# Kernel tuning notes

Hardware: AMD Instinct MI355X
Metric: run time of the kernel (lower is better)

The kernel has to match this reference:

```python
import jax, jax.numpy as jnp
import numpy as np

NUM_HEADS = 16
HEAD_DIM = 64
HIDDEN = NUM_HEADS * HEAD_DIM
LN_EPS = 1e-6


def setup_inputs() -> dict:
    key = jax.random.key(0)
    ks = jax.random.split(key, 5)
    B, T, H = 2, 2048, HIDDEN
    s = 1.0 / np.sqrt(H)
    return {
        "h": jax.random.normal(ks[0], (B, T, H), jnp.float32),
        "Wq": jax.random.normal(ks[1], (H, H), jnp.float32) * s,
        "bq": jnp.zeros((H,), jnp.float32),
        "Wk": jax.random.normal(ks[2], (H, H), jnp.float32) * s,
        "bk": jnp.zeros((H,), jnp.float32),
        "Wv": jax.random.normal(ks[3], (H, H), jnp.float32) * s,
        "bv": jnp.zeros((H,), jnp.float32),
        "Wo": jax.random.normal(ks[4], (H, H), jnp.float32) * s,
        "bo": jnp.zeros((H,), jnp.float32),
        "gamma": jnp.ones((H,), jnp.float32),
        "beta": jnp.zeros((H,), jnp.float32),
    }


def _split_heads(x):
    B, T, H = x.shape
    return x.reshape(B, T, NUM_HEADS, HEAD_DIM).transpose(0, 2, 1, 3)  # [B,h,T,d]


def reference(h, Wq, bq, Wk, bk, Wv, bv, Wo, bo, gamma, beta):
    # QKV projections (nn.Linear: x @ W^T + b)
    Q = _split_heads(h @ Wq.T + bq)
    K = _split_heads(h @ Wk.T + bk)
    V = _split_heads(h @ Wv.T + bv)
    scale = HEAD_DIM ** -0.5
    scores = jnp.einsum("bhqd,bhkd->bhqk", Q, K) * scale  # [B,h,T,T]
    attn = jax.nn.softmax(scores, axis=-1)
    ctx = jnp.einsum("bhqk,bhkd->bhqd", attn, V)          # [B,h,T,d]
    B, _, T, _ = ctx.shape
    ctx = ctx.transpose(0, 2, 1, 3).reshape(B, T, HIDDEN)
    out = ctx @ Wo.T + bo + h  # dropout is identity at eval
    # LayerNorm(eps=1e-6)
    mu = out.mean(-1, keepdims=True)
    var = jnp.mean((out - mu) ** 2, -1, keepdims=True)
    return (out - mu) * jax.lax.rsqrt(var + LN_EPS) * gamma + beta
```

## Files before the change

### kernel.cpp

```cpp
#include <hip/hip_runtime.h>
#include <hip/hip_bf16.h>

#define NH   16
#define HD   64
#define HID  1024
#define TSEQ 2048
#define BATCH 2
#define KSCALE 0.18033688011112042f

typedef __attribute__((ext_vector_type(4))) float f32x4;
typedef __attribute__((ext_vector_type(8))) short s16x8;
typedef __attribute__((ext_vector_type(4))) short s16x4;
typedef __attribute__((ext_vector_type(8))) _Float16 f16x8;

__device__ __forceinline__ unsigned short f2bf(float f) {
  union { float f; unsigned int u; } v; v.f = f;
  unsigned int r = v.u + 0x7fffu + ((v.u >> 16) & 1u);
  return (unsigned short)(r >> 16);
}
__device__ __forceinline__ float bf2f(unsigned short b) {
  union { unsigned int u; float f; } v; v.u = ((unsigned int)b) << 16; return v.f;
}

__device__ __forceinline__ void async_cp16(const unsigned short* g, unsigned short* l) {
  __builtin_amdgcn_global_load_lds(
      (const __attribute__((address_space(1))) unsigned int*)g,
      (__attribute__((address_space(3))) unsigned int*)l, 16, 0, 0);
}

__global__ __launch_bounds__(256) void cast_all_k(
    const float* __restrict__ h,
    const float* __restrict__ w0, const float* __restrict__ w1,
    const float* __restrict__ w2, const float* __restrict__ w3,
    unsigned short* __restrict__ hb, unsigned short* __restrict__ wbase) {
  int i = blockIdx.x * 256 + threadIdx.x;
  const float* src; unsigned short* dst; int idx; float sc = 1.f;
  if (i < 1048576) { src = h; dst = hb; idx = i; }
  else {
    int idx4 = i - 1048576;
    int w = idx4 >> 18;
    idx = idx4 & 262143;
    src = (w == 0) ? w0 : (w == 1) ? w1 : (w == 2) ? w2 : w3;
    dst = wbase + (size_t)(idx4 - idx) * 4;
    if (w == 1) sc = KSCALE;
  }
  float4 v = ((const float4*)src)[idx];
  ushort4 o;
  o.x = f2bf(v.x * sc); o.y = f2bf(v.y * sc); o.z = f2bf(v.z * sc); o.w = f2bf(v.w * sc);
  ((ushort4*)dst)[idx] = o;
}

__device__ __forceinline__ void gemm_core(const unsigned short* __restrict__ Ag,
                                          const unsigned short* __restrict__ Bg,
                                          unsigned short* Ash, unsigned short* Bsh,
                                          f32x4 acc[4][4]) {
  const int tid  = threadIdx.x;
  const int lane = tid & 63;
  const int wave = tid >> 6;
  const int l15  = lane & 15;
  const int quad = lane >> 4;
  const int wm   = (wave >> 1) * 64;
  const int wn   = (wave & 1) * 64;
  const int idx0 = tid * 8;
  const int idx1 = idx0 + 2048;
  const int r0 = idx0 >> 5, c0 = idx0 & 31;
  const int r1 = idx1 >> 5, c1 = idx1 & 31;
#pragma unroll
  for (int i = 0; i < 4; ++i)
#pragma unroll
    for (int j = 0; j < 4; ++j) acc[i][j] = f32x4{0.f, 0.f, 0.f, 0.f};

  for (int k0 = 0; k0 < HID; k0 += 32) {
    __syncthreads();
    async_cp16(Ag + r0 * HID + k0 + c0, Ash + idx0);
    async_cp16(Ag + r1 * HID + k0 + c1, Ash + idx1);
    async_cp16(Bg + r0 * HID + k0 + c0, Bsh + idx0);
    async_cp16(Bg + r1 * HID + k0 + c1, Bsh + idx1);
    __syncthreads();
    s16x8 af[4], bfr[4];
#pragma unroll
    for (int i = 0; i < 4; ++i)
      af[i] = *(const s16x8*)(Ash + (wm + i * 16 + l15) * 32 + quad * 8);
#pragma unroll
    for (int j = 0; j < 4; ++j)
      bfr[j] = *(const s16x8*)(Bsh + (wn + j * 16 + l15) * 32 + quad * 8);
#pragma unroll
    for (int i = 0; i < 4; ++i)
#pragma unroll
      for (int j = 0; j < 4; ++j)
        acc[i][j] = __builtin_amdgcn_mfma_f32_16x16x32_bf16(af[i], bfr[j], acc[i][j], 0, 0, 0);
  }
}

__global__ __launch_bounds__(256) void gemm_qkv(
    const unsigned short* __restrict__ hb,
    const unsigned short* __restrict__ wq, const unsigned short* __restrict__ wk,
    const unsigned short* __restrict__ wv,
    const float* __restrict__ bq, const float* __restrict__ bk, const float* __restrict__ bv,
    unsigned short* __restrict__ qo, unsigned short* __restrict__ ko,
    unsigned short* __restrict__ vto) {
  __shared__ unsigned short Ash[128 * 32];
  __shared__ unsigned short Bsh[128 * 32];
  const unsigned short* Bw; const float* bias; float bsc = 1.f;
  if (blockIdx.z == 0)      { Bw = wq; bias = bq; }
  else if (blockIdx.z == 1) { Bw = wk; bias = bk; bsc = KSCALE; }
  else                      { Bw = wv; bias = bv; }
  const int bm = blockIdx.y * 128, bn = blockIdx.x * 128;
  f32x4 acc[4][4];
  gemm_core(hb + (size_t)bm * HID, Bw + (size_t)bn * HID, Ash, Bsh, acc);

  const int tid = threadIdx.x, lane = tid & 63, wave = tid >> 6;
  const int l15 = lane & 15, quad = lane >> 4;
  const int wm = (wave >> 1) * 64, wn = (wave & 1) * 64;
  if (blockIdx.z == 2) {
#pragma unroll
    for (int j = 0; j < 4; ++j) {
      const int col = bn + wn + j * 16 + l15;
      const float bb = bias[col];
      const int head = col >> 6, d = col & 63;
#pragma unroll
      for (int i = 0; i < 4; ++i) {
        const int row0 = bm + wm + i * 16 + quad * 4;
        const int bI = row0 >> 11, t0 = row0 & 2047;
        unsigned short o[4];
#pragma unroll
        for (int r = 0; r < 4; ++r) {
          _Float16 hv = (_Float16)(acc[i][j][r] + bb);
          o[r] = __builtin_bit_cast(unsigned short, hv);
        }
        *(s16x4*)(vto + ((size_t)((bI * NH + head) * HD + d)) * TSEQ + t0) = *(const s16x4*)o;
      }
    }
  } else {
    unsigned short* outp = (blockIdx.z == 0) ? qo : ko;
#pragma unroll
    for (int j = 0; j < 4; ++j) {
      const int col = bn + wn + j * 16 + l15;
      const float bb = bias[col] * bsc;
      const int head = col >> 6, d = col & 63;
#pragma unroll
      for (int i = 0; i < 4; ++i) {
#pragma unroll
        for (int r = 0; r < 4; ++r) {
          const int row = bm + wm + i * 16 + quad * 4 + r;
          const int bI = row >> 11, t = row & 2047;
          outp[(((size_t)(bI * NH + head) * TSEQ) + t) * HD + d] = f2bf(acc[i][j][r] + bb);
        }
      }
    }
  }
}

__global__ __launch_bounds__(256) void gemm_out(
    const unsigned short* __restrict__ ctx, const unsigned short* __restrict__ wo,
    const float* __restrict__ bo, const float* __restrict__ hres,
    float* __restrict__ outf) {
  __shared__ unsigned short Ash[128 * 32];
  __shared__ unsigned short Bsh[64 * 32];
  const int tid = threadIdx.x, lane = tid & 63, wave = tid >> 6;
  const int l15 = lane & 15, quad = lane >> 4;
  const int wm = (wave >> 1) * 64, wn = (wave & 1) * 32;
  const int bm = blockIdx.y * 128, bn = blockIdx.x * 64;
  const unsigned short* Ag = ctx + (size_t)bm * HID;
  const unsigned short* Bg = wo + (size_t)bn * HID;
  const int idx0 = tid * 8, idx1 = idx0 + 2048;
  const int r0 = idx0 >> 5, c0 = idx0 & 31;
  const int r1 = idx1 >> 5, c1 = idx1 & 31;
  f32x4 acc[4][2];
#pragma unroll
  for (int i = 0; i < 4; ++i)
#pragma unroll
    for (int j = 0; j < 2; ++j) acc[i][j] = f32x4{0.f, 0.f, 0.f, 0.f};

  for (int k0 = 0; k0 < HID; k0 += 32) {
    __syncthreads();
    async_cp16(Ag + r0 * HID + k0 + c0, Ash + idx0);
    async_cp16(Ag + r1 * HID + k0 + c1, Ash + idx1);
    async_cp16(Bg + r0 * HID + k0 + c0, Bsh + idx0);
    __syncthreads();
    s16x8 af[4], bfr[2];
#pragma unroll
    for (int i = 0; i < 4; ++i)
      af[i] = *(const s16x8*)(Ash + (wm + i * 16 + l15) * 32 + quad * 8);
#pragma unroll
    for (int j = 0; j < 2; ++j)
      bfr[j] = *(const s16x8*)(Bsh + (wn + j * 16 + l15) * 32 + quad * 8);
#pragma unroll
    for (int i = 0; i < 4; ++i)
#pragma unroll
      for (int j = 0; j < 2; ++j)
        acc[i][j] = __builtin_amdgcn_mfma_f32_16x16x32_bf16(af[i], bfr[j], acc[i][j], 0, 0, 0);
  }
#pragma unroll
  for (int j = 0; j < 2; ++j) {
    const int col = bn + wn + j * 16 + l15;
    const float bb = bo[col];
#pragma unroll
    for (int i = 0; i < 4; ++i) {
#pragma unroll
      for (int r = 0; r < 4; ++r) {
        const int row = bm + wm + i * 16 + quad * 4 + r;
        const size_t off = (size_t)row * HID + col;
        outf[off] = acc[i][j][r] + bb + hres[off];
      }
    }
  }
}

__global__ __launch_bounds__(256, 2) void attn_k(
    const unsigned short* __restrict__ qb, const unsigned short* __restrict__ kb,
    const unsigned short* __restrict__ vt, unsigned short* __restrict__ ctx,
    unsigned short* __restrict__ Opart, float* __restrict__ rsumP,
    int split, int ntiles) {
  __shared__ unsigned short Ksh[64 * 72];
  __shared__ unsigned short Vsh[64 * 72];
  __shared__ unsigned short Psh[4][32 * 72];

  const int tid = threadIdx.x, lane = tid & 63, wave = tid >> 6;
  const int l15 = lane & 15, quad = lane >> 4;
  const int z = blockIdx.z;
  const int b = split ? (z >> 1) : z;
  const int half = split ? (z & 1) : 0;
  const int h = blockIdx.y, qt = blockIdx.x;
  const size_t ho = ((size_t)(b * NH + h)) * TSEQ * HD;
  const unsigned short* Qh = qb + ho;
  const unsigned short* Kh = kb + ho;
  const unsigned short* Vh = vt + ho;
  const int q0 = qt * 128 + wave * 32;
  const int kt0 = half * ntiles;

  s16x8 qf[2][2];
#pragma unroll
  for (int s = 0; s < 2; ++s)
#pragma unroll
    for (int ks = 0; ks < 2; ++ks)
      qf[s][ks] = *(const s16x8*)(Qh + (size_t)(q0 + s * 16 + l15) * HD + ks * 32 + quad * 8);

  f32x4 accO[2][4];
  float rsum[2][4];
#pragma unroll
  for (int s = 0; s < 2; ++s) {
#pragma unroll
    for (int n = 0; n < 4; ++n) accO[s][n] = f32x4{0.f, 0.f, 0.f, 0.f};
#pragma unroll
    for (int r = 0; r < 4; ++r) rsum[s][r] = 0.f;
  }

  const int sr = tid >> 3, sc = (tid & 7) * 8;
  s16x8 kreg[2], vreg[2];
#pragma unroll
  for (int hf = 0; hf < 2; ++hf) {
    kreg[hf] = *(const s16x8*)(Kh + (size_t)(kt0 * 64 + sr + hf * 32) * HD + sc);
    vreg[hf] = *(const s16x8*)(Vh + (size_t)(sr + hf * 32) * TSEQ + kt0 * 64 + sc);
  }

  for (int kt = 0; kt < ntiles; ++kt) {
    __syncthreads();
#pragma unroll
    for (int hf = 0; hf < 2; ++hf) {
      *(s16x8*)(Ksh + (sr + hf * 32) * 72 + sc) = kreg[hf];
      *(s16x8*)(Vsh + (sr + hf * 32) * 72 + sc) = vreg[hf];
    }
    __syncthreads();
    if (kt + 1 < ntiles) {
      const int k0n = (kt0 + kt + 1) * 64;
#pragma unroll
      for (int hf = 0; hf < 2; ++hf) {
        kreg[hf] = *(const s16x8*)(Kh + (size_t)(k0n + sr + hf * 32) * HD + sc);
        vreg[hf] = *(const s16x8*)(Vh + (size_t)(sr + hf * 32) * TSEQ + k0n + sc);
      }
    }

    f32x4 accS[2][4];
#pragma unroll
    for (int s = 0; s < 2; ++s)
#pragma unroll
      for (int n = 0; n < 4; ++n) accS[s][n] = f32x4{0.f, 0.f, 0.f, 0.f};
#pragma unroll
    for (int ks = 0; ks < 2; ++ks) {
#pragma unroll
      for (int n = 0; n < 4; ++n) {
        s16x8 bk = *(const s16x8*)(Ksh + (n * 16 + l15) * 72 + ks * 32 + quad * 8);
#pragma unroll
        for (int s = 0; s < 2; ++s)
          accS[s][n] = __builtin_amdgcn_mfma_f32_16x16x32_bf16(qf[s][ks], bk, accS[s][n], 0, 0, 0);
      }
    }

    unsigned short* Pw = Psh[wave];
#pragma unroll
    for (int s = 0; s < 2; ++s)
#pragma unroll
      for (int n = 0; n < 4; ++n)
#pragma unroll
        for (int r = 0; r < 4; ++r) {
          float e = exp2f(accS[s][n][r]);
          rsum[s][r] += e;
          _Float16 he = (_Float16)e;
          Pw[(s * 16 + quad * 4 + r) * 72 + n * 16 + l15] = __builtin_bit_cast(unsigned short, he);
        }

    f16x8 vf[2][4];
#pragma unroll
    for (int ks = 0; ks < 2; ++ks)
#pragma unroll
      for (int n = 0; n < 4; ++n)
        vf[ks][n] = *(const f16x8*)(Vsh + (n * 16 + l15) * 72 + ks * 32 + quad * 8);

    asm volatile("s_waitcnt lgkmcnt(0)" ::: "memory");

    f16x8 pf[2][2];
#pragma unroll
    for (int s = 0; s < 2; ++s)
#pragma unroll
      for (int ks = 0; ks < 2; ++ks)
        pf[s][ks] = *(const f16x8*)(Pw + (s * 16 + l15) * 72 + ks * 32 + quad * 8);
#pragma unroll
    for (int ks = 0; ks < 2; ++ks)
#pragma unroll
      for (int n = 0; n < 4; ++n)
#pragma unroll
        for (int s = 0; s < 2; ++s)
          accO[s][n] = __builtin_amdgcn_mfma_f32_16x16x32_f16(pf[s][ks], vf[ks][n], accO[s][n], 0, 0, 0);
  }

#pragma unroll
  for (int s = 0; s < 2; ++s)
#pragma unroll
    for (int r = 0; r < 4; ++r) {
      float t = rsum[s][r];
#pragma unroll
      for (int off = 1; off < 16; off <<= 1) t += __shfl_xor(t, off, 64);
      rsum[s][r] = t;
    }

  if (split) {
    const size_t ob = ((size_t)((half * BATCH + b) * NH + h)) * TSEQ * HD;
#pragma unroll
    for (int s = 0; s < 2; ++s)
#pragma unroll
      for (int n = 0; n < 4; ++n) {
        const int d = n * 16 + l15;
#pragma unroll
        for (int r = 0; r < 4; ++r) {
          const int t = q0 + s * 16 + quad * 4 + r;
          Opart[ob + (size_t)t * HD + d] = f2bf(accO[s][n][r]);
        }
      }
    if (l15 == 0) {
      const size_t rb = ((size_t)((half * BATCH + b) * NH + h)) * TSEQ;
#pragma unroll
      for (int s = 0; s < 2; ++s)
#pragma unroll
        for (int r = 0; r < 4; ++r)
          rsumP[rb + q0 + s * 16 + quad * 4 + r] = rsum[s][r];
    }
  } else {
#pragma unroll
    for (int s = 0; s < 2; ++s)
#pragma unroll
      for (int n = 0; n < 4; ++n) {
        const int d = n * 16 + l15;
#pragma unroll
        for (int r = 0; r < 4; ++r) {
          const int t = q0 + s * 16 + quad * 4 + r;
          ctx[((size_t)(b * TSEQ + t)) * HID + h * HD + d] = f2bf(accO[s][n][r] / rsum[s][r]);
        }
      }
  }
}

__global__ __launch_bounds__(256) void combine_k(
    const unsigned short* __restrict__ Opart, const float* __restrict__ rsumP,
    unsigned short* __restrict__ ctx) {
  const int gtid = blockIdx.x * 256 + threadIdx.x;
  const int d = (gtid & 7) * 8;
  const int rem = gtid >> 3;
  const int t = rem & 2047;
  const int bh = rem >> 11;
  const size_t offA = ((size_t)bh * TSEQ + t) * HD + d;
  const size_t offB = ((size_t)(32 + bh) * TSEQ + t) * HD + d;
  s16x8 a = *(const s16x8*)(Opart + offA);
  s16x8 c = *(const s16x8*)(Opart + offB);
  const float ra = rsumP[(size_t)bh * TSEQ + t];
  const float rb = rsumP[(size_t)(32 + bh) * TSEQ + t];
  const float inv = 1.f / (ra + rb);
  unsigned short o[8];
#pragma unroll
  for (int j = 0; j < 8; ++j)
    o[j] = f2bf((bf2f(((const unsigned short*)&a)[j]) + bf2f(((const unsigned short*)&c)[j])) * inv);
  const int b = bh >> 4, h = bh & 15;
  *(s16x8*)(ctx + ((size_t)(b * TSEQ + t)) * HID + h * HD + d) = *(const s16x8*)o;
}

__global__ __launch_bounds__(256) void ln_k(float* __restrict__ io,
                                            const float* __restrict__ gamma,
                                            const float* __restrict__ beta) {
  const int row = blockIdx.x, tid = threadIdx.x;
  float x[4]; float s = 0.f, s2 = 0.f;
#pragma unroll
  for (int i = 0; i < 4; ++i) {
    x[i] = io[(size_t)row * HID + tid + i * 256];
    s += x[i]; s2 += x[i] * x[i];
  }
#pragma unroll
  for (int off = 1; off < 64; off <<= 1) {
    s  += __shfl_xor(s, off, 64);
    s2 += __shfl_xor(s2, off, 64);
  }
  __shared__ float red[8];
  const int wave = tid >> 6;
  if ((tid & 63) == 0) { red[wave] = s; red[wave + 4] = s2; }
  __syncthreads();
  s  = red[0] + red[1] + red[2] + red[3];
  s2 = red[4] + red[5] + red[6] + red[7];
  const float mean = s * (1.f / HID);
  const float var  = s2 * (1.f / HID) - mean * mean;
  const float rstd = rsqrtf(var + 1e-6f);
#pragma unroll
  for (int i = 0; i < 4; ++i) {
    const int col = tid + i * 256;
    io[(size_t)row * HID + col] = (x[i] - mean) * rstd * gamma[col] + beta[col];
  }
}

extern "C" void kernel_launch(void* const* d_in, const int* in_sizes, int n_in,
                              void* d_out, int out_size, void* d_ws, size_t ws_size,
                              hipStream_t stream) {
  const float* h    = (const float*)d_in[0];
  const float* Wq   = (const float*)d_in[1];
  const float* bq   = (const float*)d_in[2];
  const float* Wk   = (const float*)d_in[3];
  const float* bk   = (const float*)d_in[4];
  const float* Wv   = (const float*)d_in[5];
  const float* bv   = (const float*)d_in[6];
  const float* Wo   = (const float*)d_in[7];
  const float* bo   = (const float*)d_in[8];
  const float* gamma = (const float*)d_in[9];
  const float* beta  = (const float*)d_in[10];
  float* out = (float*)d_out;

  unsigned short* hb   = (unsigned short*)d_ws;
  unsigned short* wqb  = hb  + 4194304;
  unsigned short* wkb  = wqb + 1048576;
  unsigned short* wvb  = wkb + 1048576;
  unsigned short* wob  = wvb + 1048576;
  unsigned short* qb   = wob + 1048576;
  unsigned short* kb   = qb  + 4194304;
  unsigned short* vtf  = kb  + 4194304;
  unsigned short* Opart = vtf + 4194304;
  float*          rsumP = (float*)(Opart + 8388608);
  unsigned short* ctxb = hb;

  const size_t need = (size_t)(28 * 1024 * 1024) * 2 + 131072 * 4;
  const int split = (ws_size >= need) ? 1 : 0;

  cast_all_k<<<8192, 256, 0, stream>>>(h, Wq, Wk, Wv, Wo, hb, wqb);
  gemm_qkv<<<dim3(8, 32, 3), 256, 0, stream>>>(hb, wqb, wkb, wvb, bq, bk, bv, qb, kb, vtf);
  if (split) {
    attn_k<<<dim3(TSEQ / 128, NH, BATCH * 2), 256, 0, stream>>>(qb, kb, vtf, ctxb, Opart, rsumP, 1, 16);
    combine_k<<<2048, 256, 0, stream>>>(Opart, rsumP, ctxb);
  } else {
    attn_k<<<dim3(TSEQ / 128, NH, BATCH), 256, 0, stream>>>(qb, kb, vtf, ctxb, Opart, rsumP, 0, 32);
  }
  gemm_out<<<dim3(16, 32), 256, 0, stream>>>(ctxb, wob, bo, h, out);
  ln_k<<<4096, 256, 0, stream>>>(out, gamma, beta);
}
```

Measured before the change: 244.4 us.

## Compute transposed scores so P stays in registers as MFMA operand

The attention kernel swaps the MFMA operand order to compute S^T. Each lane's exp'd fp16 probabilities then form a direct B-operand for 16x16x16 f16 MFMAs, which removes the per-wave P shared-memory round trip and its waitcnt. The change also reduces the row-sum shuffles, and the output is now written as packed 4-element vector stores. In exchange it issues twice as many smaller-K MFMAs for PV and adds a different V fragment read pattern from LDS.

```diff
diff --git a/kernel.cpp b/kernel.cpp
--- a/kernel.cpp
+++ b/kernel.cpp
@@ -12,6 +12,7 @@
 typedef __attribute__((ext_vector_type(8))) short s16x8;
 typedef __attribute__((ext_vector_type(4))) short s16x4;
 typedef __attribute__((ext_vector_type(8))) _Float16 f16x8;
+typedef __attribute__((ext_vector_type(4))) _Float16 f16x4;
 
 __device__ __forceinline__ unsigned short f2bf(float f) {
   union { float f; unsigned int u; } v; v.f = f;
@@ -214,7 +215,6 @@
     int split, int ntiles) {
   __shared__ unsigned short Ksh[64 * 72];
   __shared__ unsigned short Vsh[64 * 72];
-  __shared__ unsigned short Psh[4][32 * 72];
 
   const int tid = threadIdx.x, lane = tid & 63, wave = tid >> 6;
   const int l15 = lane & 15, quad = lane >> 4;
@@ -236,15 +236,13 @@
     for (int ks = 0; ks < 2; ++ks)
       qf[s][ks] = *(const s16x8*)(Qh + (size_t)(q0 + s * 16 + l15) * HD + ks * 32 + quad * 8);
 
-  f32x4 accO[2][4];
-  float rsum[2][4];
-#pragma unroll
-  for (int s = 0; s < 2; ++s) {
-#pragma unroll
-    for (int n = 0; n < 4; ++n) accO[s][n] = f32x4{0.f, 0.f, 0.f, 0.f};
-#pragma unroll
-    for (int r = 0; r < 4; ++r) rsum[s][r] = 0.f;
-  }
+  f32x4 accO[4][2];
+  float rsum[2];
+#pragma unroll
+  for (int n2 = 0; n2 < 4; ++n2)
+#pragma unroll
+    for (int s = 0; s < 2; ++s) accO[n2][s] = f32x4{0.f, 0.f, 0.f, 0.f};
+  rsum[0] = rsum[1] = 0.f;
 
   const int sr = tid >> 3, sc = (tid & 7) * 8;
   s16x8 kreg[2], vreg[2];
@@ -280,93 +278,80 @@
     for (int ks = 0; ks < 2; ++ks) {
 #pragma unroll
       for (int n = 0; n < 4; ++n) {
-        s16x8 bk = *(const s16x8*)(Ksh + (n * 16 + l15) * 72 + ks * 32 + quad * 8);
+        s16x8 kf = *(const s16x8*)(Ksh + (n * 16 + l15) * 72 + ks * 32 + quad * 8);
 #pragma unroll
         for (int s = 0; s < 2; ++s)
-          accS[s][n] = __builtin_amdgcn_mfma_f32_16x16x32_bf16(qf[s][ks], bk, accS[s][n], 0, 0, 0);
-      }
-    }
-
-    unsigned short* Pw = Psh[wave];
+          accS[s][n] = __builtin_amdgcn_mfma_f32_16x16x32_bf16(kf, qf[s][ks], accS[s][n], 0, 0, 0);
+      }
+    }
+
+    f16x4 pB[2][4];
 #pragma unroll
     for (int s = 0; s < 2; ++s)
 #pragma unroll
-      for (int n = 0; n < 4; ++n)
-#pragma unroll
-        for (int r = 0; r < 4; ++r) {
-          float e = exp2f(accS[s][n][r]);
-          rsum[s][r] += e;
-          _Float16 he = (_Float16)e;
-          Pw[(s * 16 + quad * 4 + r) * 72 + n * 16 + l15] = __builtin_bit_cast(unsigned short, he);
-        }
-
-    f16x8 vf[2][4];
-#pragma unroll
-    for (int ks = 0; ks < 2; ++ks)
-#pragma unroll
-      for (int n = 0; n < 4; ++n)
-        vf[ks][n] = *(const f16x8*)(Vsh + (n * 16 + l15) * 72 + ks * 32 + quad * 8);
-
-    asm volatile("s_waitcnt lgkmcnt(0)" ::: "memory");
-
-    f16x8 pf[2][2];
-#pragma unroll
-    for (int s = 0; s < 2; ++s)
-#pragma unroll
-      for (int ks = 0; ks < 2; ++ks)
-        pf[s][ks] = *(const f16x8*)(Pw + (s * 16 + l15) * 72 + ks * 32 + quad * 8);
-#pragma unroll
-    for (int ks = 0; ks < 2; ++ks)
-#pragma unroll
-      for (int n = 0; n < 4; ++n)
+      for (int n = 0; n < 4; ++n) {
+        float e0 = exp2f(accS[s][n][0]);
+        float e1 = exp2f(accS[s][n][1]);
+        float e2 = exp2f(accS[s][n][2]);
+        float e3 = exp2f(accS[s][n][3]);
+        rsum[s] += (e0 + e1) + (e2 + e3);
+        pB[s][n] = f16x4{(_Float16)e0, (_Float16)e1, (_Float16)e2, (_Float16)e3};
+      }
+
+#pragma unroll
+    for (int n = 0; n < 4; ++n) {
+#pragma unroll
+      for (int n2 = 0; n2 < 4; ++n2) {
+        f16x4 vA = *(const f16x4*)(Vsh + (n2 * 16 + l15) * 72 + n * 16 + quad * 4);
 #pragma unroll
         for (int s = 0; s < 2; ++s)
-          accO[s][n] = __builtin_amdgcn_mfma_f32_16x16x32_f16(pf[s][ks], vf[ks][n], accO[s][n], 0, 0, 0);
-  }
-
-#pragma unroll
-  for (int s = 0; s < 2; ++s)
-#pragma unroll
-    for (int r = 0; r < 4; ++r) {
-      float t = rsum[s][r];
-#pragma unroll
-      for (int off = 1; off < 16; off <<= 1) t += __shfl_xor(t, off, 64);
-      rsum[s][r] = t;
-    }
+          accO[n2][s] = __builtin_amdgcn_mfma_f32_16x16x16f16(vA, pB[s][n], accO[n2][s], 0, 0, 0);
+      }
+    }
+  }
+
+#pragma unroll
+  for (int s = 0; s < 2; ++s) {
+    float t = rsum[s];
+    t += __shfl_xor(t, 16, 64);
+    t += __shfl_xor(t, 32, 64);
+    rsum[s] = t;
+  }
 
   if (split) {
     const size_t ob = ((size_t)((half * BATCH + b) * NH + h)) * TSEQ * HD;
 #pragma unroll
-    for (int s = 0; s < 2; ++s)
-#pragma unroll
-      for (int n = 0; n < 4; ++n) {
-        const int d = n * 16 + l15;
-#pragma unroll
-        for (int r = 0; r < 4; ++r) {
-          const int t = q0 + s * 16 + quad * 4 + r;
-          Opart[ob + (size_t)t * HD + d] = f2bf(accO[s][n][r]);
-        }
-      }
-    if (l15 == 0) {
+    for (int s = 0; s < 2; ++s) {
+      const int t = q0 + s * 16 + l15;
+#pragma unroll
+      for (int n2 = 0; n2 < 4; ++n2) {
+        const int d0 = n2 * 16 + quad * 4;
+        unsigned short o[4];
+#pragma unroll
+        for (int r = 0; r < 4; ++r) o[r] = f2bf(accO[n2][s][r]);
+        *(s16x4*)(Opart + ob + (size_t)t * HD + d0) = *(const s16x4*)o;
+      }
+    }
+    if (quad == 0) {
       const size_t rb = ((size_t)((half * BATCH + b) * NH + h)) * TSEQ;
 #pragma unroll
       for (int s = 0; s < 2; ++s)
-#pragma unroll
-        for (int r = 0; r < 4; ++r)
-          rsumP[rb + q0 + s * 16 + quad * 4 + r] = rsum[s][r];
+        rsumP[rb + q0 + s * 16 + l15] = rsum[s];
     }
   } else {
 #pragma unroll
-    for (int s = 0; s < 2; ++s)
-#pragma unroll
-      for (int n = 0; n < 4; ++n) {
-        const int d = n * 16 + l15;
-#pragma unroll
-        for (int r = 0; r < 4; ++r) {
-          const int t = q0 + s * 16 + quad * 4 + r;
-          ctx[((size_t)(b * TSEQ + t)) * HID + h * HD + d] = f2bf(accO[s][n][r] / rsum[s][r]);
-        }
-      }
+    for (int s = 0; s < 2; ++s) {
+      const int t = q0 + s * 16 + l15;
+      const float inv = 1.f / rsum[s];
+#pragma unroll
+      for (int n2 = 0; n2 < 4; ++n2) {
+        const int d0 = n2 * 16 + quad * 4;
+        unsigned short o[4];
+#pragma unroll
+        for (int r = 0; r < 4; ++r) o[r] = f2bf(accO[n2][s][r] * inv);
+        *(s16x4*)(ctx + ((size_t)(b * TSEQ + t)) * HID + h * HD + d0) = *(const s16x4*)o;
+      }
+    }
   }
 }
 
```

New measurement: 238.0 us. -2.6%, faster.
